# Optimization experiments

Measured on AMD Instinct MI355X. Metric: run time of the kernel, lower is better.

The kernel has to match this reference:

```python
import jax, jax.numpy as jnp
import numpy as np

NUM_BLOCKS = 8
BLOCK_SIZE = 96
HIDDEN_FACTOR = 1
B, H, W = 1, 360, 181


def setup_inputs() -> dict:
    key = jax.random.key(0)
    k_inp, k_w, k_b = jax.random.split(key, 3)
    out_size = BLOCK_SIZE * HIDDEN_FACTOR
    inp = jax.random.normal(k_inp, (B, NUM_BLOCKS, BLOCK_SIZE, H, W, 2), dtype=jnp.float32)
    weight = jax.random.normal(k_w, (NUM_BLOCKS, BLOCK_SIZE, out_size, 2), dtype=jnp.float32) * 0.02
    bias = jax.random.normal(k_b, (NUM_BLOCKS, out_size, 1, 1, 2), dtype=jnp.float32) * 0.02
    return {"inp": inp, "weight": weight, "bias": bias}


def reference(inp, weight, bias):
    # inp:    [b, k, i, x, y, 2]  (last dim = real/imag)
    # weight: [k, i, o, 2]; bias: [k, o, 1, 1, 2]
    ar, ai = inp[..., 0], inp[..., 1]
    wr, wi = weight[..., 0], weight[..., 1]
    # complex matmul: (ar + i*ai) @ (wr + i*wi), block-diagonal over k
    real = jnp.einsum("bkixy,kio->bkoxy", ar, wr) - jnp.einsum("bkixy,kio->bkoxy", ai, wi)
    imag = jnp.einsum("bkixy,kio->bkoxy", ai, wr) + jnp.einsum("bkixy,kio->bkoxy", ar, wi)
    return jnp.stack([real, imag], axis=-1) + bias  # [b, k, o, x, y, 2]
```

## Files before the change

kernel.cpp:

```cpp
#include <hip/hip_runtime.h>

#define XY 65160
#define NI 96
#define NO 96
#define NK 8
#define NT 510

typedef __attribute__((ext_vector_type(8))) short short8;
typedef __attribute__((ext_vector_type(4))) float floatx4;

union FragU { short8 v; unsigned u[4]; };

static __device__ __forceinline__ unsigned cvt_pk(float lo, float hi) {
    unsigned r;
    asm("v_cvt_pk_bf16_f32 %0, %1, %2" : "=v"(r) : "v"(lo), "v"(hi));
    return r;
}

__global__ __launch_bounds__(512, 4) void cmult_kernel(
    const float* __restrict__ inp, const float* __restrict__ weight,
    const float* __restrict__ bias, float* __restrict__ out)
{
    __shared__ unsigned wlds[36 * 64 * 4];
    __shared__ float2 blds[NO];

    const int tid  = threadIdx.x;
    const int lane = tid & 63;
    const int wave = tid >> 6;
    const int k    = blockIdx.y;
    const int l15  = lane & 15;
    const int quad = lane >> 4;

    const float* wk   = weight + (size_t)k * NI * NO * 2;
    const float* inpk = inp    + (size_t)k * NI * XY * 2;

    for (int idx = tid; idx < NI * NO; idx += 512) {
        int i = idx / NO;
        int o = idx - i * NO;
        float2 w = *reinterpret_cast<const float2*>(wk + (size_t)idx * 2);
        int s = i >> 4, q = (i >> 2) & 3, t = i & 3;
        int m = o >> 4, c = o & 15;
        wlds[((s * 6 + m) * 64 + (q * 16 + c)) * 4 + t] = cvt_pk(w.x, w.y);
    }
    if (tid < NO) {
        blds[tid] = *reinterpret_cast<const float2*>(bias + ((size_t)k * NO + tid) * 2);
    }
    __syncthreads();

    for (int tidx = blockIdx.x; tidx < NT; tidx += gridDim.x) {
        int xy  = tidx * 128 + wave * 16 + l15;
        int xyc = xy < XY ? xy : XY - 1;

        floatx4 accR[6], accI[6];
        #pragma unroll
        for (int m = 0; m < 6; ++m) {
            accR[m] = (floatx4){0.f,0.f,0.f,0.f};
            accI[m] = (floatx4){0.f,0.f,0.f,0.f};
        }

        #pragma unroll
        for (int s = 0; s < 6; ++s) {
            FragU bN, bS;
            #pragma unroll
            for (int t = 0; t < 4; ++t) {
                int i = 16 * s + 4 * quad + t;
                float2 a = *reinterpret_cast<const float2*>(inpk + ((size_t)i * XY + xyc) * 2);
                unsigned p = cvt_pk(a.x, a.y);
                bN.u[t] = p ^ 0x80000000u;
                bS.u[t] = (p >> 16) | (p << 16);
            }
            #pragma unroll
            for (int m = 0; m < 6; ++m) {
                FragU wf;
                uint4 wp = *(reinterpret_cast<const uint4*>(wlds) + (s * 6 + m) * 64 + lane);
                wf.u[0] = wp.x; wf.u[1] = wp.y; wf.u[2] = wp.z; wf.u[3] = wp.w;
                accR[m] = __builtin_amdgcn_mfma_f32_16x16x32_bf16(wf.v, bN.v, accR[m], 0, 0, 0);
                accI[m] = __builtin_amdgcn_mfma_f32_16x16x32_bf16(wf.v, bS.v, accI[m], 0, 0, 0);
            }
        }

        if (xy < XY) {
            #pragma unroll
            for (int m = 0; m < 6; ++m) {
                #pragma unroll
                for (int r = 0; r < 4; ++r) {
                    int o = 16 * m + 4 * quad + r;
                    float2 b = blds[o];
                    float2 ov;
                    ov.x = accR[m][r] + b.x;
                    ov.y = accI[m][r] + b.y;
                    *reinterpret_cast<float2*>(out + ((size_t)(k * NO + o) * XY + xy) * 2) = ov;
                }
            }
        }
    }
}

extern "C" void kernel_launch(void* const* d_in, const int* in_sizes, int n_in,
                              void* d_out, int out_size, void* d_ws, size_t ws_size,
                              hipStream_t stream)
{
    const float* inp    = (const float*)d_in[0];
    const float* weight = (const float*)d_in[1];
    const float* bias   = (const float*)d_in[2];
    float* out = (float*)d_out;

    dim3 grid(128, NK), block(512);
    hipLaunchKernelGGL(cmult_kernel, grid, block, 0, stream, inp, weight, bias, out);
}
```

Measured before the change: 796.9 us.

## Stage input tiles in LDS via global_load_lds and keep weights in registers

Each tile of 64 spatial points across all 96 input channels is now copied into LDS with coalesced 16-byte global_load_lds transfers, replacing scattered 8-byte per-lane global loads. The bf16 weight fragments are preloaded into registers instead of being read from LDS. The block's waves are split into two output-channel halves and four spatial groups. This is meant to improve global read coalescing and remove the LDS weight traffic. In exchange it adds two barriers per tile with no double buffering, and uses more registers for the weights.

```diff
diff --git a/kernel.cpp b/kernel.cpp
--- a/kernel.cpp
+++ b/kernel.cpp
@@ -4,12 +4,16 @@
 #define NI 96
 #define NO 96
 #define NK 8
-#define NT 510
+#define TNX 64
+#define NT 1019
 
 typedef __attribute__((ext_vector_type(8))) short short8;
 typedef __attribute__((ext_vector_type(4))) float floatx4;
 
 union FragU { short8 v; unsigned u[4]; };
+
+typedef __attribute__((address_space(3))) unsigned       lds_u32;
+typedef const __attribute__((address_space(1))) unsigned g_u32;
 
 static __device__ __forceinline__ unsigned cvt_pk(float lo, float hi) {
     unsigned r;
@@ -21,41 +25,61 @@
     const float* __restrict__ inp, const float* __restrict__ weight,
     const float* __restrict__ bias, float* __restrict__ out)
 {
-    __shared__ unsigned wlds[36 * 64 * 4];
+    __shared__ float atile[NI * TNX * 2];
     __shared__ float2 blds[NO];
 
     const int tid  = threadIdx.x;
     const int lane = tid & 63;
     const int wave = tid >> 6;
+    const int h    = wave & 1;
+    const int g    = wave >> 1;
     const int k    = blockIdx.y;
     const int l15  = lane & 15;
     const int quad = lane >> 4;
 
+    const float* inpk = inp    + (size_t)k * NI * XY * 2;
     const float* wk   = weight + (size_t)k * NI * NO * 2;
-    const float* inpk = inp    + (size_t)k * NI * XY * 2;
 
-    for (int idx = tid; idx < NI * NO; idx += 512) {
-        int i = idx / NO;
-        int o = idx - i * NO;
-        float2 w = *reinterpret_cast<const float2*>(wk + (size_t)idx * 2);
-        int s = i >> 4, q = (i >> 2) & 3, t = i & 3;
-        int m = o >> 4, c = o & 15;
-        wlds[((s * 6 + m) * 64 + (q * 16 + c)) * 4 + t] = cvt_pk(w.x, w.y);
+    if (tid < NO) blds[tid] = *reinterpret_cast<const float2*>(bias + ((size_t)k * NO + tid) * 2);
+
+    FragU wfr[6][3];
+    #pragma unroll
+    for (int s = 0; s < 6; ++s) {
+        #pragma unroll
+        for (int mm = 0; mm < 3; ++mm) {
+            int m = 3 * h + mm;
+            #pragma unroll
+            for (int t = 0; t < 4; ++t) {
+                int i = 16 * s + 4 * quad + t;
+                float2 w = *reinterpret_cast<const float2*>(wk + ((size_t)i * NO + 16 * m + l15) * 2);
+                wfr[s][mm].u[t] = cvt_pk(w.x, w.y);
+            }
+        }
     }
-    if (tid < NO) {
-        blds[tid] = *reinterpret_cast<const float2*>(bias + ((size_t)k * NO + tid) * 2);
-    }
-    __syncthreads();
 
     for (int tidx = blockIdx.x; tidx < NT; tidx += gridDim.x) {
-        int xy  = tidx * 128 + wave * 16 + l15;
-        int xyc = xy < XY ? xy : XY - 1;
+        const int x0 = tidx * TNX;
 
-        floatx4 accR[6], accI[6];
+        __syncthreads();
+
         #pragma unroll
-        for (int m = 0; m < 6; ++m) {
-            accR[m] = (floatx4){0.f,0.f,0.f,0.f};
-            accI[m] = (floatx4){0.f,0.f,0.f,0.f};
+        for (int j = 0; j < 6; ++j) {
+            int n   = wave * 6 + j;
+            int row = 2 * n + (lane >> 5);
+            int xy  = x0 + (lane & 31) * 2;
+            if (xy > XY - 2) xy = XY - 2;
+            const float* gsrc = inpk + ((size_t)row * XY + xy) * 2;
+            __builtin_amdgcn_global_load_lds(
+                (g_u32*)gsrc, (lds_u32*)atile + n * 256, 16, 0, 0);
+        }
+
+        __syncthreads();
+
+        floatx4 accR[3], accI[3];
+        #pragma unroll
+        for (int mm = 0; mm < 3; ++mm) {
+            accR[mm] = (floatx4){0.f,0.f,0.f,0.f};
+            accI[mm] = (floatx4){0.f,0.f,0.f,0.f};
         }
 
         #pragma unroll
@@ -64,31 +88,29 @@
             #pragma unroll
             for (int t = 0; t < 4; ++t) {
                 int i = 16 * s + 4 * quad + t;
-                float2 a = *reinterpret_cast<const float2*>(inpk + ((size_t)i * XY + xyc) * 2);
+                float2 a = *reinterpret_cast<const float2*>(atile + ((size_t)i * TNX + g * 16 + l15) * 2);
                 unsigned p = cvt_pk(a.x, a.y);
                 bN.u[t] = p ^ 0x80000000u;
                 bS.u[t] = (p >> 16) | (p << 16);
             }
             #pragma unroll
-            for (int m = 0; m < 6; ++m) {
-                FragU wf;
-                uint4 wp = *(reinterpret_cast<const uint4*>(wlds) + (s * 6 + m) * 64 + lane);
-                wf.u[0] = wp.x; wf.u[1] = wp.y; wf.u[2] = wp.z; wf.u[3] = wp.w;
-                accR[m] = __builtin_amdgcn_mfma_f32_16x16x32_bf16(wf.v, bN.v, accR[m], 0, 0, 0);
-                accI[m] = __builtin_amdgcn_mfma_f32_16x16x32_bf16(wf.v, bS.v, accI[m], 0, 0, 0);
+            for (int mm = 0; mm < 3; ++mm) {
+                accR[mm] = __builtin_amdgcn_mfma_f32_16x16x32_bf16(wfr[s][mm].v, bN.v, accR[mm], 0, 0, 0);
+                accI[mm] = __builtin_amdgcn_mfma_f32_16x16x32_bf16(wfr[s][mm].v, bS.v, accI[mm], 0, 0, 0);
             }
         }
 
+        int xy = x0 + g * 16 + l15;
         if (xy < XY) {
             #pragma unroll
-            for (int m = 0; m < 6; ++m) {
+            for (int mm = 0; mm < 3; ++mm) {
                 #pragma unroll
                 for (int r = 0; r < 4; ++r) {
-                    int o = 16 * m + 4 * quad + r;
+                    int o = 16 * (3 * h + mm) + 4 * quad + r;
                     float2 b = blds[o];
                     float2 ov;
-                    ov.x = accR[m][r] + b.x;
-                    ov.y = accI[m][r] + b.y;
+                    ov.x = accR[mm][r] + b.x;
+                    ov.y = accI[mm][r] + b.y;
                     *reinterpret_cast<float2*>(out + ((size_t)(k * NO + o) * XY + xy) * 2) = ov;
                 }
             }
```

After: 839.2 us. 1.05x slower.
